# Kernel optimization log

Hardware: AMD Instinct MI355X
Metric: run time of the kernel (lower is better)

## Reference

```python
import jax, jax.numpy as jnp
import numpy as np

NEG_SLOPE = 0.2  # PyG GATConv default negative_slope
N_NODES = 10000
N_EDGES = 320000
IN_CH = 512
HID = 128
HEADS = 4
N_CLASSES = 2


def gat_conv(x, src, dst, n, W, att_src, att_dst, bias, concat):
    """PyG-style GATConv (shared weights for src/dst, eval mode: no dropout)."""
    H, C = att_src.shape
    h = (x @ W).reshape(-1, H, C)                      # [N, H, C]
    a_src = jnp.sum(h * att_src[None], axis=-1)        # [N, H]
    a_dst = jnp.sum(h * att_dst[None], axis=-1)        # [N, H]
    e = a_src[src] + a_dst[dst]                        # [E, H]
    e = jnp.where(e > 0, e, NEG_SLOPE * e)             # LeakyReLU
    # numerically stable softmax over incoming edges of each dst node
    m = jax.ops.segment_max(e, dst, num_segments=n)    # [N, H]
    m = jnp.where(jnp.isfinite(m), m, 0.0)
    ex = jnp.exp(e - m[dst])
    denom = jax.ops.segment_sum(ex, dst, num_segments=n)
    alpha = ex / (denom[dst] + 1e-16)                  # [E, H]
    out = jax.ops.segment_sum(alpha[:, :, None] * h[src], dst, num_segments=n)  # [N,H,C]
    if concat:
        out = out.reshape(n, H * C)
    else:
        out = out.mean(axis=1)
    return out + bias


def setup_inputs() -> dict:
    key = jax.random.key(0)
    ks = jax.random.split(key, 8)
    x = jax.random.normal(ks[0], (N_NODES, IN_CH), dtype=jnp.float32)
    edge_index = jax.random.randint(ks[1], (2, N_EDGES), 0, N_NODES, dtype=jnp.int32)
    s1 = 1.0 / np.sqrt(IN_CH)
    s2 = 1.0 / np.sqrt(HEADS * HID)
    return {
        "x": x,
        "edge_index": edge_index,
        "W1": jax.random.normal(ks[2], (IN_CH, HEADS * HID), dtype=jnp.float32) * s1,
        "att_src1": jax.random.normal(ks[3], (HEADS, HID), dtype=jnp.float32) * s2,
        "att_dst1": jax.random.normal(ks[4], (HEADS, HID), dtype=jnp.float32) * s2,
        "b1": jnp.zeros((HEADS * HID,), dtype=jnp.float32),
        "W2": jax.random.normal(ks[5], (HEADS * HID, N_CLASSES), dtype=jnp.float32) * s2,
        "att_src2": jax.random.normal(ks[6], (1, N_CLASSES), dtype=jnp.float32),
        "att_dst2": jax.random.normal(ks[7], (1, N_CLASSES), dtype=jnp.float32),
        "b2": jnp.zeros((N_CLASSES,), dtype=jnp.float32),
    }


def reference(x, edge_index, W1, att_src1, att_dst1, b1, W2, att_src2, att_dst2, b2):
    n = x.shape[0]
    loop = jnp.arange(n, dtype=edge_index.dtype)       # PyG add_self_loops=True
    src = jnp.concatenate([edge_index[0], loop])
    dst = jnp.concatenate([edge_index[1], loop])
    h = gat_conv(x, src, dst, n, W1, att_src1, att_dst1, b1, concat=True)
    h = jax.nn.elu(h)
    out = gat_conv(h, src, dst, n, W2, att_src2, att_dst2, b2, concat=False)
    return out
```

## Files before the change

kernel.cpp:

```cpp
#include <hip/hip_runtime.h>
#include <hip/hip_bf16.h>

#define N_NODES 10000
#define N_EDGES 320000
#define E_TOT   330000
#define IN_CH   512
#define F1      512
#define HID     128
#define HEADS   4
#define SLOTS   128

typedef __attribute__((ext_vector_type(8))) short bf16x8;
typedef __attribute__((ext_vector_type(4))) float f32x4;

__device__ __forceinline__ float lo16(unsigned u) { return __uint_as_float(u << 16); }
__device__ __forceinline__ float hi16(unsigned u) { return __uint_as_float(u & 0xffff0000u); }
__device__ __forceinline__ unsigned short bfbits(float f) {
    __hip_bfloat16 h = __float2bfloat16(f);
    return *(unsigned short*)&h;
}

__device__ __forceinline__ void gload_lds16(const void* g, void* l) {
    __builtin_amdgcn_global_load_lds(
        (const __attribute__((address_space(1))) unsigned int*)g,
        (__attribute__((address_space(3))) unsigned int*)l, 16, 0, 0);
}

__global__ void k_prep(const float* __restrict__ x, unsigned short* __restrict__ xb,
                       const float* __restrict__ w1, unsigned short* __restrict__ w1t,
                       int* __restrict__ zbase,
                       const int* __restrict__ src, const int* __restrict__ dst,
                       int* __restrict__ cnt, int* __restrict__ slots) {
    __shared__ float tile[64][65];
    int b = blockIdx.x;
    int t = threadIdx.x;
    if (b < 5000) {
        int idx = b * 256 + t;
        float4 v = ((const float4*)x)[idx];
        ushort4 u;
        u.x = bfbits(v.x); u.y = bfbits(v.y); u.z = bfbits(v.z); u.w = bfbits(v.w);
        ((ushort4*)xb)[idx] = u;
    } else if (b < 5064) {
        int bb = b - 5000;
        int bi = bb >> 3, bj = bb & 7;
        int r0 = t >> 6, col = t & 63;
#pragma unroll
        for (int p = 0; p < 16; ++p) {
            int row = p * 4 + r0;
            tile[row][col] = w1[(size_t)(bi * 64 + row) * 512 + bj * 64 + col];
        }
        __syncthreads();
#pragma unroll
        for (int p = 0; p < 16; ++p) {
            int row = p * 4 + r0;
            w1t[(size_t)(bj * 64 + row) * 512 + bi * 64 + col] = bfbits(tile[col][row]);
        }
    } else if (b < 5533) {
        int idx = (b - 5064) * 256 + t;
        if (idx < 120000) zbase[idx] = 0;
    } else {
        int e = (b - 5533) * 256 + t;
        if (e < E_TOT) {
            int d, s;
            if (e < N_EDGES) { d = dst[e]; s = src[e]; } else { d = e - N_EDGES; s = d; }
            int pos = atomicAdd(&cnt[d], 1);
            if (pos < SLOTS) slots[d * SLOTS + pos] = s;
        }
    }
}

__device__ __forceinline__ void gemm_step(const __hip_bfloat16* A, const __hip_bfloat16* B,
                                          int wr, int wc, int col16, int quad,
                                          f32x4 acc[4][4]) {
#pragma unroll
    for (int kk = 0; kk < 2; ++kk) {
        bf16x8 af[4], bf[4];
#pragma unroll
        for (int m = 0; m < 4; ++m) {
            int r = wr * 64 + m * 16 + col16;
            af[m] = *(const bf16x8*)((const char*)A + r * 128 +
                                     ((kk * 64 + quad * 16) ^ ((r & 7) << 4)));
        }
#pragma unroll
        for (int c = 0; c < 4; ++c) {
            int r = wc * 64 + c * 16 + col16;
            bf[c] = *(const bf16x8*)((const char*)B + r * 128 +
                                     ((kk * 64 + quad * 16) ^ ((r & 7) << 4)));
        }
#pragma unroll
        for (int m = 0; m < 4; ++m)
#pragma unroll
            for (int c = 0; c < 4; ++c)
                acc[m][c] = __builtin_amdgcn_mfma_f32_16x16x32_bf16(af[m], bf[c], acc[m][c], 0, 0, 0);
    }
}

__global__ __launch_bounds__(256) void k_gemm1(const __hip_bfloat16* __restrict__ xb,
                                               const __hip_bfloat16* __restrict__ w1t,
                                               const float* __restrict__ as_vec,
                                               const float* __restrict__ ad_vec,
                                               __hip_bfloat16* __restrict__ h1b,
                                               float* __restrict__ a_src,
                                               float* __restrict__ a_dst) {
    __shared__ __align__(16) __hip_bfloat16 lsA[2][128 * 64];
    __shared__ __align__(16) __hip_bfloat16 lsB[2][128 * 64];
    int nt = blockIdx.x & 3;
    int mt = blockIdx.x >> 2;
    int row0 = mt * 128;
    int t = threadIdx.x;
    int lane = t & 63;
    int wid = t >> 6;
    int wr = wid >> 1, wc = wid & 1;
    int col16 = lane & 15, quad = lane >> 4;

    const __hip_bfloat16* ga[4];
    const __hip_bfloat16* gb[4];
    unsigned loff[4];
#pragma unroll
    for (int p = 0; p < 4; ++p) {
        int ci = p * 256 + t;
        int row = ci >> 3, ch = ci & 7;
        int sch = ch ^ (row & 7);
        ga[p] = xb + (size_t)min(row0 + row, N_NODES - 1) * IN_CH + sch * 8;
        gb[p] = w1t + (size_t)(nt * 128 + row) * IN_CH + sch * 8;
        loff[p] = ci * 16;
    }

    f32x4 acc[4][4] = {};

#pragma unroll
    for (int p = 0; p < 4; ++p) gload_lds16(ga[p], (char*)lsA[0] + loff[p]);
#pragma unroll
    for (int p = 0; p < 4; ++p) gload_lds16(gb[p], (char*)lsB[0] + loff[p]);
    __syncthreads();

#pragma unroll 1
    for (int s = 0; s < 7; ++s) {
        int nb = (s + 1) & 1, kt = (s + 1) * 64;
#pragma unroll
        for (int p = 0; p < 4; ++p) gload_lds16(ga[p] + kt, (char*)lsA[nb] + loff[p]);
#pragma unroll
        for (int p = 0; p < 4; ++p) gload_lds16(gb[p] + kt, (char*)lsB[nb] + loff[p]);
        gemm_step(lsA[s & 1], lsB[s & 1], wr, wc, col16, quad, acc);
        __syncthreads();
    }
    gemm_step(lsA[1], lsB[1], wr, wc, col16, quad, acc);

    float asv[4], adv[4];
#pragma unroll
    for (int c = 0; c < 4; ++c) {
        int col = nt * 128 + wc * 64 + c * 16 + col16;
        asv[c] = as_vec[col];
        adv[c] = ad_vec[col];
    }
#pragma unroll
    for (int m = 0; m < 4; ++m) {
#pragma unroll
        for (int reg = 0; reg < 4; ++reg) {
            int row = row0 + wr * 64 + m * 16 + quad * 4 + reg;
            bool ok = row < N_NODES;
            float ps = 0.f, pd = 0.f;
#pragma unroll
            for (int c = 0; c < 4; ++c) {
                float v = acc[m][c][reg];
                ps += v * asv[c];
                pd += v * adv[c];
                if (ok) h1b[(size_t)row * F1 + nt * 128 + wc * 64 + c * 16 + col16] =
                            __float2bfloat16(v);
            }
#pragma unroll
            for (int off = 1; off <= 8; off <<= 1) {
                ps += __shfl_xor(ps, off);
                pd += __shfl_xor(pd, off);
            }
            if (col16 == 0 && ok) {
                atomicAdd(&a_src[row * HEADS + nt], ps);
                atomicAdd(&a_dst[row * HEADS + nt], pd);
            }
        }
    }
}

__global__ __launch_bounds__(256) void k_aggr1(const __hip_bfloat16* __restrict__ h1b,
                                               const float* __restrict__ a_src,
                                               const float* __restrict__ a_dst,
                                               const int* __restrict__ cnt,
                                               const int* __restrict__ slots,
                                               const float* __restrict__ b1,
                                               const float* __restrict__ w2,
                                               const float* __restrict__ as2,
                                               const float* __restrict__ ad2,
                                               float* __restrict__ h2,
                                               float* __restrict__ a_src2,
                                               float* __restrict__ a_dst2) {
    int h = blockIdx.x & 3;
    int n = (blockIdx.x >> 2) * 16 + (threadIdx.x >> 4);
    int s16 = threadIdx.x & 15;
    int cn = min(cnt[n], SLOTS);
    const int* sl = slots + n * SLOTS;
    float adst = a_dst[n * HEADS + h];
    int c0 = h * 128 + s16 * 8;
    const __hip_bfloat16* hb = h1b + c0;
    float dsum = 0.f;
    float acc[8] = {};
    int nb = (cn + 7) >> 3;

    int sB[8], sC[8] = {0, 0, 0, 0, 0, 0, 0, 0};
    float avA[8], avB[8];
    uint4 dA[8], dB[8];
#pragma unroll
    for (int j = 0; j < 8; ++j) sB[j] = sl[min(j, cn - 1)];
#pragma unroll
    for (int j = 0; j < 8; ++j) avA[j] = a_src[sB[j] * HEADS + h];
#pragma unroll
    for (int j = 0; j < 8; ++j) dA[j] = *(const uint4*)(hb + (size_t)sB[j] * F1);
#pragma unroll
    for (int j = 0; j < 8; ++j) sB[j] = sl[min(8 + j, cn - 1)];

    for (int b = 0; b < nb; ++b) {
        int i = b << 3;
        bool more = (b + 1) < nb;
        if (b + 2 < nb) {
            int i2 = i + 16;
            if (i2 + 8 <= cn) {
                int4 u0 = *(const int4*)(sl + i2);
                int4 u1 = *(const int4*)(sl + i2 + 4);
                sC[0] = u0.x; sC[1] = u0.y; sC[2] = u0.z; sC[3] = u0.w;
                sC[4] = u1.x; sC[5] = u1.y; sC[6] = u1.z; sC[7] = u1.w;
            } else {
#pragma unroll
                for (int j = 0; j < 8; ++j) sC[j] = sl[min(i2 + j, cn - 1)];
            }
        }
        if (more) {
#pragma unroll
            for (int j = 0; j < 8; ++j) avB[j] = a_src[sB[j] * HEADS + h];
#pragma unroll
            for (int j = 0; j < 8; ++j) dB[j] = *(const uint4*)(hb + (size_t)sB[j] * F1);
        }
        float w[8];
#pragma unroll
        for (int j = 0; j < 8; ++j) {
            float e = avA[j] + adst;
            e = fmaxf(e, 0.2f * e);
            float ww = __expf(e);
            w[j] = (i + j < cn) ? ww : 0.f;
            dsum += w[j];
        }
#pragma unroll
        for (int j = 0; j < 8; ++j) {
            acc[0] += w[j] * lo16(dA[j].x); acc[1] += w[j] * hi16(dA[j].x);
            acc[2] += w[j] * lo16(dA[j].y); acc[3] += w[j] * hi16(dA[j].y);
            acc[4] += w[j] * lo16(dA[j].z); acc[5] += w[j] * hi16(dA[j].z);
            acc[6] += w[j] * lo16(dA[j].w); acc[7] += w[j] * hi16(dA[j].w);
        }
        if (more) {
#pragma unroll
            for (int j = 0; j < 8; ++j) { avA[j] = avB[j]; dA[j] = dB[j]; sB[j] = sC[j]; }
        }
    }
    float inv = 1.f / (dsum + 1e-16f);
    float ps0 = 0.f, ps1 = 0.f;
#pragma unroll
    for (int j = 0; j < 8; ++j) {
        float v = acc[j] * inv + b1[c0 + j];
        v = v > 0.f ? v : __expf(v) - 1.f;
        ps0 += v * w2[(c0 + j) * 2 + 0];
        ps1 += v * w2[(c0 + j) * 2 + 1];
    }
#pragma unroll
    for (int off = 1; off <= 8; off <<= 1) {
        ps0 += __shfl_xor(ps0, off);
        ps1 += __shfl_xor(ps1, off);
    }
    if (s16 == 0) {
        atomicAdd(&h2[n * 2 + 0], ps0);
        atomicAdd(&h2[n * 2 + 1], ps1);
        atomicAdd(&a_src2[n], ps0 * as2[0] + ps1 * as2[1]);
        atomicAdd(&a_dst2[n], ps0 * ad2[0] + ps1 * ad2[1]);
    }
}

__global__ __launch_bounds__(256) void k_aggr2(const float* __restrict__ h2,
                                               const float* __restrict__ a_src2,
                                               const float* __restrict__ a_dst2,
                                               const int* __restrict__ cnt,
                                               const int* __restrict__ slots,
                                               const float* __restrict__ b2,
                                               float* __restrict__ out) {
    int lane = threadIdx.x & 63;
    int sub = lane >> 4, slot = lane & 15;
    int n = blockIdx.x * 16 + (threadIdx.x >> 6) * 4 + sub;
    int cn = min(cnt[n], SLOTS);
    const int* sl = slots + n * SLOTS;
    float adst = a_dst2[n];
    float dsum = 0.f, acc0 = 0.f, acc1 = 0.f;
    for (int i = slot; i < cn; i += 16) {
        int s = sl[i];
        float e = a_src2[s] + adst;
        e = fmaxf(e, 0.2f * e);
        float w = __expf(e);
        dsum += w;
        acc0 += w * h2[s * 2 + 0];
        acc1 += w * h2[s * 2 + 1];
    }
#pragma unroll
    for (int off = 1; off <= 8; off <<= 1) {
        dsum += __shfl_xor(dsum, off);
        acc0 += __shfl_xor(acc0, off);
        acc1 += __shfl_xor(acc1, off);
    }
    if (slot == 0) {
        float inv = 1.f / (dsum + 1e-16f);
        out[n * 2 + 0] = acc0 * inv + b2[0];
        out[n * 2 + 1] = acc1 * inv + b2[1];
    }
}

extern "C" void kernel_launch(void* const* d_in, const int* in_sizes, int n_in,
                              void* d_out, int out_size, void* d_ws, size_t ws_size,
                              hipStream_t stream) {
    const float* x   = (const float*)d_in[0];
    const int*   ei  = (const int*)d_in[1];
    const float* W1  = (const float*)d_in[2];
    const float* as1 = (const float*)d_in[3];
    const float* ad1 = (const float*)d_in[4];
    const float* b1  = (const float*)d_in[5];
    const float* W2  = (const float*)d_in[6];
    const float* as2 = (const float*)d_in[7];
    const float* ad2 = (const float*)d_in[8];
    const float* b2  = (const float*)d_in[9];

    char* ws = (char*)d_ws;
    __hip_bfloat16* h1b = (__hip_bfloat16*)(ws);
    __hip_bfloat16* xb  = (__hip_bfloat16*)(ws + 10240000);
    __hip_bfloat16* w1t = (__hip_bfloat16*)(ws + 20480000);
    const size_t S = 21004288;
    float* a_src1 = (float*)(ws + S);
    float* a_dst1 = (float*)(ws + S + 160000);
    float* h2     = (float*)(ws + S + 320000);
    float* a_src2 = (float*)(ws + S + 400000);
    float* a_dst2 = (float*)(ws + S + 440000);
    int*   cnt    = (int*)(ws + S + 480000);
    int*   slots  = (int*)(ws + S + 520000);

    const int* srcArr = ei;
    const int* dstArr = ei + N_EDGES;

    hipMemsetAsync(cnt, 0, N_NODES * sizeof(int), stream);
    k_prep<<<5533 + 1290, 256, 0, stream>>>(x, (unsigned short*)xb, W1,
                                            (unsigned short*)w1t, (int*)a_src1,
                                            srcArr, dstArr, cnt, slots);
    k_gemm1<<<316, 256, 0, stream>>>(xb, w1t, as1, ad1, h1b, a_src1, a_dst1);
    k_aggr1<<<2500, 256, 0, stream>>>(h1b, a_src1, a_dst1, cnt, slots, b1,
                                      W2, as2, ad2, h2, a_src2, a_dst2);
    k_aggr2<<<N_NODES / 16, 256, 0, stream>>>(h2, a_src2, a_dst2, cnt, slots, b2,
                                              (float*)d_out);
}
```

Measured before the change: 185.9 us.

## Move edge bucketing into GEMM launch and widen per-node aggregation parallelism

```diff
diff --git a/kernel.cpp b/kernel.cpp
--- a/kernel.cpp
+++ b/kernel.cpp
@@ -28,9 +28,7 @@
 
 __global__ void k_prep(const float* __restrict__ x, unsigned short* __restrict__ xb,
                        const float* __restrict__ w1, unsigned short* __restrict__ w1t,
-                       int* __restrict__ zbase,
-                       const int* __restrict__ src, const int* __restrict__ dst,
-                       int* __restrict__ cnt, int* __restrict__ slots) {
+                       int* __restrict__ zbase) {
     __shared__ float tile[64][65];
     int b = blockIdx.x;
     int t = threadIdx.x;
@@ -55,20 +53,13 @@
             int row = p * 4 + r0;
             w1t[(size_t)(bj * 64 + row) * 512 + bi * 64 + col] = bfbits(tile[col][row]);
         }
-    } else if (b < 5533) {
+    } else {
         int idx = (b - 5064) * 256 + t;
-        if (idx < 120000) zbase[idx] = 0;
-    } else {
-        int e = (b - 5533) * 256 + t;
-        if (e < E_TOT) {
-            int d, s;
-            if (e < N_EDGES) { d = dst[e]; s = src[e]; } else { d = e - N_EDGES; s = d; }
-            int pos = atomicAdd(&cnt[d], 1);
-            if (pos < SLOTS) slots[d * SLOTS + pos] = s;
-        }
-    }
-}
-
+        if (idx < 130000) zbase[idx] = 0;
+    }
+}
+
+#define GEMM_BLKS 316
 __device__ __forceinline__ void gemm_step(const __hip_bfloat16* A, const __hip_bfloat16* B,
                                           int wr, int wc, int col16, int quad,
                                           f32x4 acc[4][4]) {
@@ -101,7 +92,21 @@
                                                const float* __restrict__ ad_vec,
                                                __hip_bfloat16* __restrict__ h1b,
                                                float* __restrict__ a_src,
-                                               float* __restrict__ a_dst) {
+                                               float* __restrict__ a_dst,
+                                               const int* __restrict__ src,
+                                               const int* __restrict__ dst,
+                                               int* __restrict__ cnt,
+                                               int* __restrict__ slots) {
+    if (blockIdx.x >= GEMM_BLKS) {
+        int e = (blockIdx.x - GEMM_BLKS) * 256 + threadIdx.x;
+        if (e < E_TOT) {
+            int d, s;
+            if (e < N_EDGES) { d = dst[e]; s = src[e]; } else { d = e - N_EDGES; s = d; }
+            int pos = atomicAdd(&cnt[d], 1);
+            if (pos < SLOTS) slots[d * SLOTS + pos] = s;
+        }
+        return;
+    }
     __shared__ __align__(16) __hip_bfloat16 lsA[2][128 * 64];
     __shared__ __align__(16) __hip_bfloat16 lsB[2][128 * 64];
     int nt = blockIdx.x & 3;
@@ -194,71 +199,88 @@
                                                float* __restrict__ a_src2,
                                                float* __restrict__ a_dst2) {
     int h = blockIdx.x & 3;
-    int n = (blockIdx.x >> 2) * 16 + (threadIdx.x >> 4);
-    int s16 = threadIdx.x & 15;
+    int n = (blockIdx.x >> 2) * 4 + (threadIdx.x >> 6);
+    int lane = threadIdx.x & 63;
+    int q = lane >> 4;
+    int c16 = lane & 15;
     int cn = min(cnt[n], SLOTS);
     const int* sl = slots + n * SLOTS;
     float adst = a_dst[n * HEADS + h];
-    int c0 = h * 128 + s16 * 8;
+    int c0 = h * 128 + c16 * 8;
     const __hip_bfloat16* hb = h1b + c0;
+
     float dsum = 0.f;
     float acc[8] = {};
-    int nb = (cn + 7) >> 3;
-
-    int sB[8], sC[8] = {0, 0, 0, 0, 0, 0, 0, 0};
-    float avA[8], avB[8];
-    uint4 dA[8], dB[8];
-#pragma unroll
-    for (int j = 0; j < 8; ++j) sB[j] = sl[min(j, cn - 1)];
-#pragma unroll
-    for (int j = 0; j < 8; ++j) avA[j] = a_src[sB[j] * HEADS + h];
-#pragma unroll
-    for (int j = 0; j < 8; ++j) dA[j] = *(const uint4*)(hb + (size_t)sB[j] * F1);
-#pragma unroll
-    for (int j = 0; j < 8; ++j) sB[j] = sl[min(8 + j, cn - 1)];
-
-    for (int b = 0; b < nb; ++b) {
-        int i = b << 3;
-        bool more = (b + 1) < nb;
-        if (b + 2 < nb) {
-            int i2 = i + 16;
-            if (i2 + 8 <= cn) {
-                int4 u0 = *(const int4*)(sl + i2);
-                int4 u1 = *(const int4*)(sl + i2 + 4);
-                sC[0] = u0.x; sC[1] = u0.y; sC[2] = u0.z; sC[3] = u0.w;
-                sC[4] = u1.x; sC[5] = u1.y; sC[6] = u1.z; sC[7] = u1.w;
-            } else {
-#pragma unroll
-                for (int j = 0; j < 8; ++j) sC[j] = sl[min(i2 + j, cn - 1)];
-            }
-        }
-        if (more) {
-#pragma unroll
-            for (int j = 0; j < 8; ++j) avB[j] = a_src[sB[j] * HEADS + h];
-#pragma unroll
-            for (int j = 0; j < 8; ++j) dB[j] = *(const uint4*)(hb + (size_t)sB[j] * F1);
-        }
-        float w[8];
+
+    int s0[8], s1[8];
+    float av0[8], av1[8];
+    uint4 d0[8], d1[8];
+    bool two = cn > 32;
+#pragma unroll
+    for (int j = 0; j < 8; ++j) s0[j] = sl[min(j * 4 + q, cn - 1)];
+#pragma unroll
+    for (int j = 0; j < 8; ++j) av0[j] = a_src[s0[j] * HEADS + h];
+#pragma unroll
+    for (int j = 0; j < 8; ++j) d0[j] = *(const uint4*)(hb + (size_t)s0[j] * F1);
+    if (two) {
+#pragma unroll
+        for (int j = 0; j < 8; ++j) s1[j] = sl[min(32 + j * 4 + q, cn - 1)];
+#pragma unroll
+        for (int j = 0; j < 8; ++j) av1[j] = a_src[s1[j] * HEADS + h];
+#pragma unroll
+        for (int j = 0; j < 8; ++j) d1[j] = *(const uint4*)(hb + (size_t)s1[j] * F1);
+    }
+#pragma unroll
+    for (int j = 0; j < 8; ++j) {
+        float e = av0[j] + adst;
+        e = fmaxf(e, 0.2f * e);
+        float w = (j * 4 + q < cn) ? __expf(e) : 0.f;
+        dsum += w;
+        acc[0] += w * lo16(d0[j].x); acc[1] += w * hi16(d0[j].x);
+        acc[2] += w * lo16(d0[j].y); acc[3] += w * hi16(d0[j].y);
+        acc[4] += w * lo16(d0[j].z); acc[5] += w * hi16(d0[j].z);
+        acc[6] += w * lo16(d0[j].w); acc[7] += w * hi16(d0[j].w);
+    }
+    if (two) {
 #pragma unroll
         for (int j = 0; j < 8; ++j) {
-            float e = avA[j] + adst;
+            float e = av1[j] + adst;
             e = fmaxf(e, 0.2f * e);
-            float ww = __expf(e);
-            w[j] = (i + j < cn) ? ww : 0.f;
-            dsum += w[j];
-        }
+            float w = (32 + j * 4 + q < cn) ? __expf(e) : 0.f;
+            dsum += w;
+            acc[0] += w * lo16(d1[j].x); acc[1] += w * hi16(d1[j].x);
+            acc[2] += w * lo16(d1[j].y); acc[3] += w * hi16(d1[j].y);
+            acc[4] += w * lo16(d1[j].z); acc[5] += w * hi16(d1[j].z);
+            acc[6] += w * lo16(d1[j].w); acc[7] += w * hi16(d1[j].w);
+        }
+    }
+    for (int i = 64; i < cn; i += 32) {
+        int ss[8]; float av[8]; uint4 dd[8];
+#pragma unroll
+        for (int j = 0; j < 8; ++j) ss[j] = sl[min(i + j * 4 + q, cn - 1)];
+#pragma unroll
+        for (int j = 0; j < 8; ++j) av[j] = a_src[ss[j] * HEADS + h];
+#pragma unroll
+        for (int j = 0; j < 8; ++j) dd[j] = *(const uint4*)(hb + (size_t)ss[j] * F1);
 #pragma unroll
         for (int j = 0; j < 8; ++j) {
-            acc[0] += w[j] * lo16(dA[j].x); acc[1] += w[j] * hi16(dA[j].x);
-            acc[2] += w[j] * lo16(dA[j].y); acc[3] += w[j] * hi16(dA[j].y);
-            acc[4] += w[j] * lo16(dA[j].z); acc[5] += w[j] * hi16(dA[j].z);
-            acc[6] += w[j] * lo16(dA[j].w); acc[7] += w[j] * hi16(dA[j].w);
-        }
-        if (more) {
-#pragma unroll
-            for (int j = 0; j < 8; ++j) { avA[j] = avB[j]; dA[j] = dB[j]; sB[j] = sC[j]; }
-        }
-    }
+            float e = av[j] + adst;
+            e = fmaxf(e, 0.2f * e);
+            float w = (i + j * 4 + q < cn) ? __expf(e) : 0.f;
+            dsum += w;
+            acc[0] += w * lo16(dd[j].x); acc[1] += w * hi16(dd[j].x);
+            acc[2] += w * lo16(dd[j].y); acc[3] += w * hi16(dd[j].y);
+            acc[4] += w * lo16(dd[j].z); acc[5] += w * hi16(dd[j].z);
+            acc[6] += w * lo16(dd[j].w); acc[7] += w * hi16(dd[j].w);
+        }
+    }
+#pragma unroll
+    for (int j = 0; j < 8; ++j) {
+        acc[j] += __shfl_xor(acc[j], 16);
+        acc[j] += __shfl_xor(acc[j], 32);
+    }
+    dsum += __shfl_xor(dsum, 16);
+    dsum += __shfl_xor(dsum, 32);
     float inv = 1.f / (dsum + 1e-16f);
     float ps0 = 0.f, ps1 = 0.f;
 #pragma unroll
@@ -273,7 +295,7 @@
         ps0 += __shfl_xor(ps0, off);
         ps1 += __shfl_xor(ps1, off);
     }
-    if (s16 == 0) {
+    if (lane == 0) {
         atomicAdd(&h2[n * 2 + 0], ps0);
         atomicAdd(&h2[n * 2 + 1], ps1);
         atomicAdd(&a_src2[n], ps0 * as2[0] + ps1 * as2[1]);
@@ -347,13 +369,13 @@
     const int* srcArr = ei;
     const int* dstArr = ei + N_EDGES;
 
-    hipMemsetAsync(cnt, 0, N_NODES * sizeof(int), stream);
-    k_prep<<<5533 + 1290, 256, 0, stream>>>(x, (unsigned short*)xb, W1,
-                                            (unsigned short*)w1t, (int*)a_src1,
-                                            srcArr, dstArr, cnt, slots);
-    k_gemm1<<<316, 256, 0, stream>>>(xb, w1t, as1, ad1, h1b, a_src1, a_dst1);
-    k_aggr1<<<2500, 256, 0, stream>>>(h1b, a_src1, a_dst1, cnt, slots, b1,
-                                      W2, as2, ad2, h2, a_src2, a_dst2);
+    k_prep<<<5064 + 508, 256, 0, stream>>>(x, (unsigned short*)xb, W1,
+                                           (unsigned short*)w1t, (int*)a_src1);
+    k_gemm1<<<GEMM_BLKS + 1290, 256, 0, stream>>>(xb, w1t, as1, ad1, h1b,
+                                                  a_src1, a_dst1,
+                                                  srcArr, dstArr, cnt, slots);
+    k_aggr1<<<N_NODES, 256, 0, stream>>>(h1b, a_src1, a_dst1, cnt, slots, b1,
+                                         W2, as2, ad2, h2, a_src2, a_dst2);
     k_aggr2<<<N_NODES / 16, 256, 0, stream>>>(h2, a_src2, a_dst2, cnt, slots, b2,
                                               (float*)d_out);
 }
```

Result: no change. 182.5 us (-1.8%).
